# Optimization experiments

Measured on AMD Instinct MI355X. Metric: run time of the kernel, lower is better.

The kernel has to match this reference:

```python
import jax, jax.numpy as jnp
import numpy as np

D_MODEL = 1024
HEADS = 4
HDIM = 64


def setup_inputs() -> dict:
    key = jax.random.key(0)
    k_x, k_qw, k_qb, k_kw, k_kb, k_hw = jax.random.split(key, 6)
    hidden_states = jax.random.normal(k_x, (2, 4096, D_MODEL), dtype=jnp.float32)
    # xavier_uniform bound for Linear(d_model -> heads*hdim)
    fan_out = HEADS * HDIM
    bound = float(np.sqrt(6.0 / (D_MODEL + fan_out)))
    q_weight = jax.random.uniform(k_qw, (fan_out, D_MODEL), minval=-bound, maxval=bound, dtype=jnp.float32)
    k_weight = jax.random.uniform(k_kw, (fan_out, D_MODEL), minval=-bound, maxval=bound, dtype=jnp.float32)
    # nn.Linear default bias init: U(-1/sqrt(fan_in), 1/sqrt(fan_in))
    b_bound = float(1.0 / np.sqrt(D_MODEL))
    q_bias = jax.random.uniform(k_qb, (fan_out,), minval=-b_bound, maxval=b_bound, dtype=jnp.float32)
    k_bias = jax.random.uniform(k_kb, (fan_out,), minval=-b_bound, maxval=b_bound, dtype=jnp.float32)
    indexer_weights = jax.random.normal(k_hw, (HEADS,), dtype=jnp.float32) * 0.1
    return {
        "hidden_states": hidden_states,
        "q_weight": q_weight,
        "q_bias": q_bias,
        "k_weight": k_weight,
        "k_bias": k_bias,
        "indexer_weights": indexer_weights,
    }


def reference(hidden_states, q_weight, q_bias, k_weight, k_bias, indexer_weights):
    b, s, _ = hidden_states.shape
    # Linear projections: x @ W^T + b  -> [b, s, heads*hdim]
    q = hidden_states @ q_weight.T + q_bias
    k = hidden_states @ k_weight.T + k_bias
    q = q.reshape(b, s, HEADS, HDIM)  # [b, s, h, d]
    k = k.reshape(b, s, HEADS, HDIM)
    # per-head QK^T -> [b, h, s, s]
    scores = jnp.einsum("bqhd,bkhd->bhqk", q, k)
    scores = jax.nn.relu(scores)
    # weighted sum over heads -> [b, s, s]
    index_scores = jnp.einsum("bhqk,h->bqk", scores, indexer_weights)
    return index_scores
```

## Files before the change

### kernel.cpp

```cpp
#include <hip/hip_runtime.h>


typedef __bf16 bf16;
typedef __bf16 bf16x4 __attribute__((ext_vector_type(4)));
typedef __bf16 bf16x8 __attribute__((ext_vector_type(8)));
typedef float f32x4 __attribute__((ext_vector_type(4)));

#define SEQ 4096
#define DMODEL 1024
#define NPROJ 256
#define MTOT 8192

__device__ __forceinline__ void async16(const void* g, void* l) {
  __builtin_amdgcn_global_load_lds(
      (const __attribute__((address_space(1))) void*)g,
      (__attribute__((address_space(3))) void*)l, 16, 0, 0);
}

__global__ __launch_bounds__(256) void k_convert(const float* __restrict__ x,
                                                 const float* __restrict__ wq,
                                                 const float* __restrict__ wk,
                                                 bf16* __restrict__ xb,
                                                 bf16* __restrict__ wqb,
                                                 bf16* __restrict__ wkb) {
  const int b = blockIdx.x, t = threadIdx.x;
  if (b < 2048) {
    int i = b * 256 + t;
#pragma unroll
    for (int r = 0; r < 4; r++) {
      float4 v = ((const float4*)x)[i + r * 524288];
      bf16x4 o = {(bf16)v.x, (bf16)v.y, (bf16)v.z, (bf16)v.w};
      ((bf16x4*)xb)[i + r * 524288] = o;
    }
  } else {
    int i = (b - 2048) * 256 + t;
#pragma unroll
    for (int r = 0; r < 2; r++) {
      float4 a = ((const float4*)wq)[i + r * 32768];
      bf16x4 oa = {(bf16)a.x, (bf16)a.y, (bf16)a.z, (bf16)a.w};
      ((bf16x4*)wqb)[i + r * 32768] = oa;
      float4 c = ((const float4*)wk)[i + r * 32768];
      bf16x4 oc = {(bf16)c.x, (bf16)c.y, (bf16)c.z, (bf16)c.w};
      ((bf16x4*)wkb)[i + r * 32768] = oc;
    }
  }
}

__global__ __launch_bounds__(256, 1) void k_proj(
    const bf16* __restrict__ xb, const bf16* __restrict__ wqb,
    const bf16* __restrict__ wkb, const float* __restrict__ qbias,
    const float* __restrict__ kbias, bf16* __restrict__ Qb,
    bf16* __restrict__ Kb) {
  __shared__ __align__(16) bf16 As[2][64 * 64];
  __shared__ __align__(16) bf16 Bs[2][256 * 64];
  const int t = threadIdx.x;
  const int lane = t & 63, w = t >> 6;
  const int m16 = lane & 15, q = lane >> 4;
  const int m0 = blockIdx.x * 64;
  const int z = blockIdx.y;
  const bf16* __restrict__ W = z ? wkb : wqb;

  f32x4 acc[4][4];
#pragma unroll
  for (int nt = 0; nt < 4; nt++)
#pragma unroll
    for (int mt = 0; mt < 4; mt++) acc[nt][mt] = {0.f, 0.f, 0.f, 0.f};

  auto stage = [&](int buf, int kt) {
#pragma unroll
    for (int p = 0; p < 2; p++) {
      int g = w * 2 + p;
      int r = g * 8 + (lane >> 3);
      int c = (lane & 7) ^ (r & 7);
      async16(xb + (size_t)(m0 + r) * DMODEL + kt * 64 + c * 8,
              As[buf] + g * 512);
    }
#pragma unroll
    for (int p = 0; p < 8; p++) {
      int g = w * 8 + p;
      int r = g * 8 + (lane >> 3);
      int c = (lane & 7) ^ (r & 7);
      async16(W + (size_t)r * DMODEL + kt * 64 + c * 8, Bs[buf] + g * 512);
    }
  };

  stage(0, 0);
  __builtin_amdgcn_s_waitcnt(0);
  __syncthreads();

  for (int kt = 0; kt < 16; kt++) {
    if (kt < 15) stage((kt + 1) & 1, kt + 1);
    const bf16* As_ = As[kt & 1];
    const bf16* Bs_ = Bs[kt & 1];
#pragma unroll
    for (int s = 0; s < 2; s++) {
      bf16x8 af[4], bx[4];
#pragma unroll
      for (int nt = 0; nt < 4; nt++) {
        int n = w * 64 + nt * 16 + m16;
        int cc = (s * 4 + q) ^ (n & 7);
        af[nt] = *(const bf16x8*)(Bs_ + n * 64 + cc * 8);
      }
#pragma unroll
      for (int mt = 0; mt < 4; mt++) {
        int m = mt * 16 + m16;
        int cc = (s * 4 + q) ^ (m & 7);
        bx[mt] = *(const bf16x8*)(As_ + m * 64 + cc * 8);
      }
#pragma unroll
      for (int nt = 0; nt < 4; nt++)
#pragma unroll
        for (int mt = 0; mt < 4; mt++)
          acc[nt][mt] = __builtin_amdgcn_mfma_f32_16x16x32_bf16(
              af[nt], bx[mt], acc[nt][mt], 0, 0, 0);
    }
    __builtin_amdgcn_s_waitcnt(0);
    __syncthreads();
  }

  const float* __restrict__ bias = z ? kbias : qbias;
  bf16* __restrict__ outp = z ? Kb : Qb;
#pragma unroll
  for (int nt = 0; nt < 4; nt++) {
    int n0 = w * 64 + nt * 16 + q * 4;
    float4 bv = *(const float4*)(bias + n0);
#pragma unroll
    for (int mt = 0; mt < 4; mt++) {
      int m = m0 + mt * 16 + m16;
      bf16x4 o = {(bf16)(acc[nt][mt][0] + bv.x), (bf16)(acc[nt][mt][1] + bv.y),
                  (bf16)(acc[nt][mt][2] + bv.z), (bf16)(acc[nt][mt][3] + bv.w)};
      *(bf16x4*)(outp + (size_t)m * NPROJ + n0) = o;
    }
  }
}

__global__ __launch_bounds__(256, 2) void k_scores(
    const bf16* __restrict__ Qb, const bf16* __restrict__ Kb,
    const float* __restrict__ iw, float* __restrict__ out) {
  __shared__ __align__(16) bf16 Ks[2][64 * 256];
  const int t = threadIdx.x;
  const int lane = t & 63, w = t >> 6;
  const int m16 = lane & 15, q = lane >> 4;

  const int bx = blockIdx.x;
  const int kq = bx & 7;
  const int strip = bx >> 3;
  const int bz = strip >> 5;
  const int q0 = (strip & 31) * 128;
  const int k0 = kq * 512;

  const float whs[4] = {iw[0], iw[1], iw[2], iw[3]};

  bf16x8 aq[2][4][2];
  {
    const bf16* qp =
        Qb + (size_t)(bz * SEQ + q0 + w * 32 + m16) * NPROJ + q * 8;
#pragma unroll
    for (int qt = 0; qt < 2; qt++)
#pragma unroll
      for (int h = 0; h < 4; h++)
#pragma unroll
        for (int j = 0; j < 2; j++)
          aq[qt][h][j] = *(const bf16x8*)(qp + (size_t)qt * 16 * NPROJ +
                                          h * 64 + j * 32);
  }

  auto stage = [&](int buf, int st) {
#pragma unroll
    for (int p = 0; p < 8; p++) {
      int g = w * 8 + p;
      int r = g * 2 + (lane >> 5);
      int c = (lane & 31) ^ (r & 31);
      async16(Kb + ((size_t)bz * SEQ + k0 + st * 64 + r) * NPROJ + c * 8,
              Ks[buf] + g * 512);
    }
  };

  stage(0, 0);
  __builtin_amdgcn_s_waitcnt(0);
  __syncthreads();

  for (int st = 0; st < 8; st++) {
    if (st < 7) stage((st + 1) & 1, st + 1);
    const bf16* KsB = Ks[st & 1];

    f32x4 accf[4][2];
#pragma unroll
    for (int kt = 0; kt < 4; kt++)
#pragma unroll
      for (int qt = 0; qt < 2; qt++) accf[kt][qt] = {0.f, 0.f, 0.f, 0.f};

#pragma unroll
    for (int h = 0; h < 4; h++) {
      const float wh = whs[h];
      bf16x8 ak[4][2];
#pragma unroll
      for (int kt = 0; kt < 4; kt++) {
        int r = kt * 16 + m16;
        const bf16* kp = KsB + r * 256;
        int c0 = (h * 8 + q) ^ (r & 31);
        int c1 = (h * 8 + 4 + q) ^ (r & 31);
        ak[kt][0] = *(const bf16x8*)(kp + c0 * 8);
        ak[kt][1] = *(const bf16x8*)(kp + c1 * 8);
      }
#pragma unroll
      for (int kt = 0; kt < 4; kt++)
#pragma unroll
        for (int qt = 0; qt < 2; qt++) {
          f32x4 tacc = {0.f, 0.f, 0.f, 0.f};
          tacc = __builtin_amdgcn_mfma_f32_16x16x32_bf16(ak[kt][0],
                                                         aq[qt][h][0], tacc,
                                                         0, 0, 0);
          tacc = __builtin_amdgcn_mfma_f32_16x16x32_bf16(ak[kt][1],
                                                         aq[qt][h][1], tacc,
                                                         0, 0, 0);
#pragma unroll
          for (int e = 0; e < 4; e++)
            accf[kt][qt][e] += wh * fmaxf(tacc[e], 0.f);
        }
    }

    __builtin_amdgcn_s_waitcnt(0);
    __syncthreads();

#pragma unroll
    for (int qt = 0; qt < 2; qt++) {
      size_t rb = ((size_t)bz * SEQ + q0 + w * 32 + qt * 16 + m16) * SEQ;
#pragma unroll
      for (int kt = 0; kt < 4; kt++) {
        int col = k0 + st * 64 + kt * 16 + q * 4;
        __builtin_nontemporal_store(accf[kt][qt], (f32x4*)(out + rb + col));
      }
    }
  }
}

extern "C" void kernel_launch(void* const* d_in, const int* in_sizes, int n_in,
                              void* d_out, int out_size, void* d_ws, size_t ws_size,
                              hipStream_t stream) {
  const float* x  = (const float*)d_in[0];
  const float* wq = (const float*)d_in[1];
  const float* qb = (const float*)d_in[2];
  const float* wk = (const float*)d_in[3];
  const float* kb = (const float*)d_in[4];
  const float* iw = (const float*)d_in[5];
  float* out = (float*)d_out;

  char* ws = (char*)d_ws;
  bf16* wqb = (bf16*)ws;
  bf16* wkb = (bf16*)(ws + 524288);
  bf16* Qb  = (bf16*)(ws + 1048576);
  bf16* Kb  = (bf16*)(ws + 1048576 + 4194304);
  bf16* xb  = (bf16*)d_out;

  k_convert<<<2176, 256, 0, stream>>>(x, wq, wk, xb, wqb, wkb);
  k_proj<<<dim3(128, 2), 256, 0, stream>>>(xb, wqb, wkb, qb, kb, Qb, Kb);
  k_scores<<<512, 256, 0, stream>>>(Qb, Kb, iw, out);
}
```

Baseline: 212.0 us.

## Fuse x fp32-to-bf16 conversion into projection GEMM and split N across blocks

The projection kernel now reads fp32 hidden states directly, converts them in registers and writes them into swizzled LDS. This removes the separate conversion pass over the 32MB input and its bf16 round trip through the output buffer. The projection's N dimension is split into two 128-column halves via a third grid dimension, doubling the block count and allowing two blocks per CU. The scores kernel switches to explicit vmcnt waits with raw barriers, overlapping the next K tile load with compute, and its output stores become regular stores instead of nontemporal ones. The risks are that each x tile is now read twice (once per N half) and that the hand-written waitcnt counts must match the actual number of outstanding loads.

Result: faster. 205.6 us (-3.0%).

```diff
diff --git a/kernel.cpp b/kernel.cpp
--- a/kernel.cpp
+++ b/kernel.cpp
@@ -17,87 +17,87 @@
       (__attribute__((address_space(3))) void*)l, 16, 0, 0);
 }
 
-__global__ __launch_bounds__(256) void k_convert(const float* __restrict__ x,
-                                                 const float* __restrict__ wq,
+#define SBAR()                                   \
+  do {                                           \
+    asm volatile("" ::: "memory");               \
+    __builtin_amdgcn_sched_barrier(0);           \
+    __builtin_amdgcn_s_barrier();                \
+    __builtin_amdgcn_sched_barrier(0);           \
+    asm volatile("" ::: "memory");               \
+  } while (0)
+
+__global__ __launch_bounds__(256) void k_convert(const float* __restrict__ wq,
                                                  const float* __restrict__ wk,
-                                                 bf16* __restrict__ xb,
                                                  bf16* __restrict__ wqb,
                                                  bf16* __restrict__ wkb) {
-  const int b = blockIdx.x, t = threadIdx.x;
-  if (b < 2048) {
-    int i = b * 256 + t;
-#pragma unroll
-    for (int r = 0; r < 4; r++) {
-      float4 v = ((const float4*)x)[i + r * 524288];
-      bf16x4 o = {(bf16)v.x, (bf16)v.y, (bf16)v.z, (bf16)v.w};
-      ((bf16x4*)xb)[i + r * 524288] = o;
-    }
-  } else {
-    int i = (b - 2048) * 256 + t;
-#pragma unroll
-    for (int r = 0; r < 2; r++) {
-      float4 a = ((const float4*)wq)[i + r * 32768];
-      bf16x4 oa = {(bf16)a.x, (bf16)a.y, (bf16)a.z, (bf16)a.w};
-      ((bf16x4*)wqb)[i + r * 32768] = oa;
-      float4 c = ((const float4*)wk)[i + r * 32768];
-      bf16x4 oc = {(bf16)c.x, (bf16)c.y, (bf16)c.z, (bf16)c.w};
-      ((bf16x4*)wkb)[i + r * 32768] = oc;
-    }
-  }
-}
-
-__global__ __launch_bounds__(256, 1) void k_proj(
-    const bf16* __restrict__ xb, const bf16* __restrict__ wqb,
+  int i = blockIdx.x * 256 + threadIdx.x;
+  float4 a = ((const float4*)wq)[i];
+  bf16x4 oa = {(bf16)a.x, (bf16)a.y, (bf16)a.z, (bf16)a.w};
+  ((bf16x4*)wqb)[i] = oa;
+  float4 b = ((const float4*)wk)[i];
+  bf16x4 ob = {(bf16)b.x, (bf16)b.y, (bf16)b.z, (bf16)b.w};
+  ((bf16x4*)wkb)[i] = ob;
+}
+
+__global__ __launch_bounds__(256, 2) void k_proj(
+    const float* __restrict__ x, const bf16* __restrict__ wqb,
     const bf16* __restrict__ wkb, const float* __restrict__ qbias,
     const float* __restrict__ kbias, bf16* __restrict__ Qb,
     bf16* __restrict__ Kb) {
   __shared__ __align__(16) bf16 As[2][64 * 64];
-  __shared__ __align__(16) bf16 Bs[2][256 * 64];
+  __shared__ __align__(16) bf16 Bs[2][128 * 64];
   const int t = threadIdx.x;
   const int lane = t & 63, w = t >> 6;
   const int m16 = lane & 15, q = lane >> 4;
   const int m0 = blockIdx.x * 64;
   const int z = blockIdx.y;
+  const int nh = blockIdx.z;
   const bf16* __restrict__ W = z ? wkb : wqb;
 
-  f32x4 acc[4][4];
-#pragma unroll
-  for (int nt = 0; nt < 4; nt++)
+  const int ar = w * 16 + (lane >> 2);
+  const int ac = (lane & 3) * 16;
+  const float* __restrict__ xrow = x + (size_t)(m0 + ar) * DMODEL + ac;
+
+  f32x4 acc[2][4];
+#pragma unroll
+  for (int nt = 0; nt < 2; nt++)
 #pragma unroll
     for (int mt = 0; mt < 4; mt++) acc[nt][mt] = {0.f, 0.f, 0.f, 0.f};
 
-  auto stage = [&](int buf, int kt) {
-#pragma unroll
-    for (int p = 0; p < 2; p++) {
-      int g = w * 2 + p;
+  float4 xv[4];
+  auto xload = [&](int kt) {
+#pragma unroll
+    for (int i = 0; i < 4; i++)
+      xv[i] = *(const float4*)(xrow + kt * 64 + i * 4);
+  };
+  auto stageB = [&](int buf, int kt) {
+#pragma unroll
+    for (int p = 0; p < 4; p++) {
+      int g = w * 4 + p;
       int r = g * 8 + (lane >> 3);
       int c = (lane & 7) ^ (r & 7);
-      async16(xb + (size_t)(m0 + r) * DMODEL + kt * 64 + c * 8,
-              As[buf] + g * 512);
-    }
-#pragma unroll
-    for (int p = 0; p < 8; p++) {
-      int g = w * 8 + p;
-      int r = g * 8 + (lane >> 3);
-      int c = (lane & 7) ^ (r & 7);
-      async16(W + (size_t)r * DMODEL + kt * 64 + c * 8, Bs[buf] + g * 512);
-    }
-  };
-
-  stage(0, 0);
-  __builtin_amdgcn_s_waitcnt(0);
-  __syncthreads();
-
-  for (int kt = 0; kt < 16; kt++) {
-    if (kt < 15) stage((kt + 1) & 1, kt + 1);
-    const bf16* As_ = As[kt & 1];
-    const bf16* Bs_ = Bs[kt & 1];
+      async16(W + (size_t)(nh * 128 + r) * DMODEL + kt * 64 + c * 8,
+              Bs[buf] + g * 512);
+    }
+  };
+  auto writeA = [&](int buf) {
+    bf16x8 o0 = {(bf16)xv[0].x, (bf16)xv[0].y, (bf16)xv[0].z, (bf16)xv[0].w,
+                 (bf16)xv[1].x, (bf16)xv[1].y, (bf16)xv[1].z, (bf16)xv[1].w};
+    bf16x8 o1 = {(bf16)xv[2].x, (bf16)xv[2].y, (bf16)xv[2].z, (bf16)xv[2].w,
+                 (bf16)xv[3].x, (bf16)xv[3].y, (bf16)xv[3].z, (bf16)xv[3].w};
+    int k0 = (lane & 3) * 2;
+    *(bf16x8*)(As[buf] + ar * 64 + ((k0) ^ (ar & 7)) * 8) = o0;
+    *(bf16x8*)(As[buf] + ar * 64 + ((k0 + 1) ^ (ar & 7)) * 8) = o1;
+  };
+  auto compute = [&](int buf) {
+    const bf16* As_ = As[buf];
+    const bf16* Bs_ = Bs[buf];
 #pragma unroll
     for (int s = 0; s < 2; s++) {
-      bf16x8 af[4], bx[4];
-#pragma unroll
-      for (int nt = 0; nt < 4; nt++) {
-        int n = w * 64 + nt * 16 + m16;
+      bf16x8 af[2], bxr[4];
+#pragma unroll
+      for (int nt = 0; nt < 2; nt++) {
+        int n = w * 32 + nt * 16 + m16;
         int cc = (s * 4 + q) ^ (n & 7);
         af[nt] = *(const bf16x8*)(Bs_ + n * 64 + cc * 8);
       }
@@ -105,31 +105,48 @@
       for (int mt = 0; mt < 4; mt++) {
         int m = mt * 16 + m16;
         int cc = (s * 4 + q) ^ (m & 7);
-        bx[mt] = *(const bf16x8*)(As_ + m * 64 + cc * 8);
-      }
-#pragma unroll
-      for (int nt = 0; nt < 4; nt++)
+        bxr[mt] = *(const bf16x8*)(As_ + m * 64 + cc * 8);
+      }
+#pragma unroll
+      for (int nt = 0; nt < 2; nt++)
 #pragma unroll
         for (int mt = 0; mt < 4; mt++)
           acc[nt][mt] = __builtin_amdgcn_mfma_f32_16x16x32_bf16(
-              af[nt], bx[mt], acc[nt][mt], 0, 0, 0);
-    }
-    __builtin_amdgcn_s_waitcnt(0);
-    __syncthreads();
-  }
+              af[nt], bxr[mt], acc[nt][mt], 0, 0, 0);
+    }
+  };
+
+  xload(0);
+  stageB(0, 0);
+  asm volatile("s_waitcnt vmcnt(4)" ::: "memory");
+  writeA(0);
+
+  for (int kt = 0; kt < 15; kt++) {
+    xload(kt + 1);
+    stageB((kt + 1) & 1, kt + 1);
+    asm volatile("s_waitcnt vmcnt(8) lgkmcnt(0)" ::: "memory");
+    SBAR();
+    compute(kt & 1);
+    asm volatile("s_waitcnt vmcnt(4)" ::: "memory");
+    writeA((kt + 1) & 1);
+    SBAR();
+  }
+  asm volatile("s_waitcnt vmcnt(0) lgkmcnt(0)" ::: "memory");
+  SBAR();
+  compute(1);
 
   const float* __restrict__ bias = z ? kbias : qbias;
   bf16* __restrict__ outp = z ? Kb : Qb;
 #pragma unroll
-  for (int nt = 0; nt < 4; nt++) {
-    int n0 = w * 64 + nt * 16 + q * 4;
-    float4 bv = *(const float4*)(bias + n0);
+  for (int nt = 0; nt < 2; nt++) {
+    int ncol = nh * 128 + w * 32 + nt * 16 + q * 4;
+    float4 bv = *(const float4*)(bias + ncol);
 #pragma unroll
     for (int mt = 0; mt < 4; mt++) {
       int m = m0 + mt * 16 + m16;
       bf16x4 o = {(bf16)(acc[nt][mt][0] + bv.x), (bf16)(acc[nt][mt][1] + bv.y),
                   (bf16)(acc[nt][mt][2] + bv.z), (bf16)(acc[nt][mt][3] + bv.w)};
-      *(bf16x4*)(outp + (size_t)m * NPROJ + n0) = o;
+      *(bf16x4*)(outp + (size_t)m * NPROJ + ncol) = o;
     }
   }
 }
@@ -177,13 +194,15 @@
   };
 
   stage(0, 0);
-  __builtin_amdgcn_s_waitcnt(0);
-  __syncthreads();
+  asm volatile("s_waitcnt vmcnt(0)" ::: "memory");
+  SBAR();
 
   for (int st = 0; st < 8; st++) {
     if (st < 7) stage((st + 1) & 1, st + 1);
+    asm volatile("s_waitcnt vmcnt(8)" ::: "memory");
+    SBAR();
+
     const bf16* KsB = Ks[st & 1];
-
     f32x4 accf[4][2];
 #pragma unroll
     for (int kt = 0; kt < 4; kt++)
@@ -220,8 +239,7 @@
         }
     }
 
-    __builtin_amdgcn_s_waitcnt(0);
-    __syncthreads();
+    SBAR();
 
 #pragma unroll
     for (int qt = 0; qt < 2; qt++) {
@@ -229,7 +247,7 @@
 #pragma unroll
       for (int kt = 0; kt < 4; kt++) {
         int col = k0 + st * 64 + kt * 16 + q * 4;
-        __builtin_nontemporal_store(accf[kt][qt], (f32x4*)(out + rb + col));
+        *(f32x4*)(out + rb + col) = accf[kt][qt];
       }
     }
   }
@@ -251,9 +269,8 @@
   bf16* wkb = (bf16*)(ws + 524288);
   bf16* Qb  = (bf16*)(ws + 1048576);
   bf16* Kb  = (bf16*)(ws + 1048576 + 4194304);
-  bf16* xb  = (bf16*)d_out;
-
-  k_convert<<<2176, 256, 0, stream>>>(x, wq, wk, xb, wqb, wkb);
-  k_proj<<<dim3(128, 2), 256, 0, stream>>>(xb, wqb, wkb, qb, kb, Qb, Kb);
+
+  k_convert<<<256, 256, 0, stream>>>(wq, wk, wqb, wkb);
+  k_proj<<<dim3(128, 2, 2), 256, 0, stream>>>(x, wqb, wkb, qb, kb, Qb, Kb);
   k_scores<<<512, 256, 0, stream>>>(Qb, Kb, iw, out);
 }
```
